# Kernel optimization log

Measured on AMD Instinct MI355X. Metric: run time of the kernel, lower is better.

The kernel has to match this reference:

```python
import jax, jax.numpy as jnp
import numpy as np

N_ITERS = 200  # matches maxIter=200 in the original QPFunction


def setup_inputs() -> dict:
    key = jax.random.key(0)
    k1, k2, k3 = jax.random.split(key, 3)
    B, M, N = 8192, 128, 64
    A = jax.random.normal(k1, (B, M, N), dtype=jnp.float32)
    x = jax.random.normal(k2, (B, N), dtype=jnp.float32)
    # b > 0 guarantees z = 0 is feasible for A z <= b, so every instance is solvable
    b = jax.random.uniform(k3, (B, M), dtype=jnp.float32)
    Q = jnp.eye(N, dtype=jnp.float32)  # module parameter: self.Q = diag(ones(feature_size))
    return {"Q": Q, "A": A, "x": x, "b": b}


def reference(Q, A, x, b):
    """Batched QP:  min_z 1/2 z^T Q z - x^T z  s.t.  A z <= b.

    Solved via FISTA (accelerated projected gradient ascent) on the dual:
        max_{lam >= 0}  -1/2 (x - A^T lam)^T Q^{-1} (x - A^T lam) - lam^T b + const
    Primal recovery: z = Q^{-1} (x - A^T lam).
    Fully batched and jit-friendly (fixed N_ITERS, lax.scan).
    """
    Qinv = jnp.linalg.inv(Q)  # [n, n], tiny

    # Lipschitz bound for dual gradient: ||A Qinv A^T||_2 <= ||A||_F^2 * ||Qinv||_F
    L = jnp.sum(A * A, axis=(1, 2)) * jnp.linalg.norm(Qinv)  # [B]
    eta = jax.lax.stop_gradient(1.0 / jnp.maximum(L, 1e-12))[:, None]  # [B, 1]

    def primal(lam):
        # z = Qinv (x - A^T lam), shape [B, n]
        return jnp.einsum('nk,bk->bn', Qinv, x - jnp.einsum('bmn,bm->bn', A, lam))

    def step(carry, _):
        lam, y, t = carry
        z = primal(y)                                   # [B, n]
        g = jnp.einsum('bmn,bn->bm', A, z) - b          # dual gradient A z - b, [B, m]
        lam_new = jax.nn.relu(y + eta * g)              # projected ascent step
        t_new = 0.5 * (1.0 + jnp.sqrt(1.0 + 4.0 * t * t))
        y_new = lam_new + ((t - 1.0) / t_new) * (lam_new - lam)
        return (lam_new, y_new, t_new), None

    lam0 = jnp.zeros_like(b)
    t0 = jnp.float32(1.0)
    (lam, _, _), _ = jax.lax.scan(step, (lam0, lam0, t0), None, length=N_ITERS)
    return primal(lam)  # optimal z, [B, n]
```

## Files before the change

kernel.cpp:

```cpp
#include <hip/hip_runtime.h>


constexpr double csqrt_(double x) {
  double g = x * 0.5 + 0.5;
  for (int i = 0; i < 40; ++i) g = 0.5 * (g + x / g);
  return g;
}
struct CoefT { float c[200]; };
constexpr CoefT make_coefs() {
  CoefT T{};
  double t = 1.0;
  for (int k = 0; k < 200; ++k) {
    double tn = 0.5 * (1.0 + csqrt_(1.0 + 4.0 * t * t));
    T.c[k] = (float)((t - 1.0) / tn);
    t = tn;
  }
  return T;
}
__device__ constexpr CoefT kCoef = make_coefs();

__device__ __forceinline__ float dpp_add_xor1(float v) {
  int r = __builtin_amdgcn_update_dpp(0, __float_as_int(v), 0xB1, 0xF, 0xF, true);
  return v + __int_as_float(r);
}
__device__ __forceinline__ float dpp_add_xor2(float v) {
  int r = __builtin_amdgcn_update_dpp(0, __float_as_int(v), 0x4E, 0xF, 0xF, true);
  return v + __int_as_float(r);
}
__device__ __forceinline__ float swz_add_xor4(float v) {
  int r = __builtin_amdgcn_ds_swizzle(__float_as_int(v), 0x101F);
  return v + __int_as_float(r);
}

__global__ __launch_bounds__(512)
void qp_fista_kernel(const float* __restrict__ A,
                     const float* __restrict__ x,
                     const float* __restrict__ b,
                     float* __restrict__ out) {
  const int batch = blockIdx.x;
  const int tid = threadIdx.x;
  const int w = tid >> 6;

  __shared__ __align__(16) float tile[8192];

  const float* Ag = A + (size_t)batch * 8192;

  {
    const float4* Ag4 = (const float4*)Ag;
    float4* t4 = (float4*)tile;
#pragma unroll
    for (int k = 0; k < 4; ++k) t4[tid + k * 512] = Ag4[tid + k * 512];
  }
  __syncthreads();

  const int r  = tid >> 2;
  const int cq = tid & 3;
  float Ar[16];
  {
    const float4* t4 = (const float4*)tile;
#pragma unroll
    for (int j = 0; j < 4; ++j) {
      float4 v = t4[r * 16 + cq * 4 + j];
      Ar[4 * j + 0] = v.x; Ar[4 * j + 1] = v.y;
      Ar[4 * j + 2] = v.z; Ar[4 * j + 3] = v.w;
    }
  }
  const int c  = tid >> 3;
  const int rq = tid & 7;
  float Ac[16];
#pragma unroll
  for (int i = 0; i < 16; ++i) Ac[i] = tile[(rq * 16 + i) * 64 + c];

  float ss = 0.f;
#pragma unroll
  for (int i = 0; i < 16; ++i) ss = fmaf(Ar[i], Ar[i], ss);
#pragma unroll
  for (int d = 1; d < 64; d <<= 1) ss += __shfl_xor(ss, d, 64);

  __syncthreads();

  float* zbuf = tile;
  float* ybuf = tile + 96;
  float* wsb  = tile + 272;

  if ((tid & 63) == 0) wsb[w] = ss;
  const float breg = b[(size_t)batch * 128 + r];
  const float xreg = x[(size_t)batch * 64 + c];
  if (rq == 0) zbuf[(c >> 4) * 20 + (c & 15)] = xreg;
  __syncthreads();

  float sum8 = 0.f;
#pragma unroll
  for (int i = 0; i < 8; ++i) sum8 += wsb[i];
  const float eta = 1.0f / fmaxf(8.0f * sum8, 1e-12f);
  const float yb0 = eta * breg;

  const float4* zs = (const float4*)(zbuf + cq * 20);
  const float4* ys = (const float4*)(ybuf + rq * 20);
  float* ywr = ybuf + w * 20 + (r & 15);
  float* zwr = zbuf + (c >> 4) * 20 + (c & 15);

  float lam = 0.f, y = 0.f;

#pragma unroll 2
  for (int it = 0; it < 199; ++it) {
    const float coef = kCoef.c[it];

    __builtin_amdgcn_s_setprio(1);
    float p0 = 0.f, p1 = 0.f;
#pragma unroll
    for (int j = 0; j < 4; ++j) {
      float4 zz = zs[j];
      p0 = fmaf(Ar[4 * j + 0], zz.x, p0);
      p1 = fmaf(Ar[4 * j + 1], zz.y, p1);
      p0 = fmaf(Ar[4 * j + 2], zz.z, p0);
      p1 = fmaf(Ar[4 * j + 3], zz.w, p1);
    }
    float acc = p0 + p1;
    acc = dpp_add_xor1(acc);
    acc = dpp_add_xor2(acc);
    float ln = fmaxf(0.f, fmaf(eta, acc, y - yb0));
    float yn = fmaf(coef, ln - lam, ln);
    __builtin_amdgcn_s_setprio(0);
    lam = ln; y = yn;
    if (cq == 0) *ywr = yn;
    __syncthreads();

    __builtin_amdgcn_s_setprio(1);
    float q0 = 0.f, q1 = 0.f;
#pragma unroll
    for (int j = 0; j < 4; ++j) {
      float4 yy = ys[j];
      q0 = fmaf(Ac[4 * j + 0], yy.x, q0);
      q1 = fmaf(Ac[4 * j + 1], yy.y, q1);
      q0 = fmaf(Ac[4 * j + 2], yy.z, q0);
      q1 = fmaf(Ac[4 * j + 3], yy.w, q1);
    }
    float s = q0 + q1;
    s = dpp_add_xor1(s);
    s = dpp_add_xor2(s);
    s = swz_add_xor4(s);
    __builtin_amdgcn_s_setprio(0);
    if (rq == 0) *zwr = xreg - s;
    __syncthreads();
  }

  {
    float p0 = 0.f, p1 = 0.f;
#pragma unroll
    for (int j = 0; j < 4; ++j) {
      float4 zz = zs[j];
      p0 = fmaf(Ar[4 * j + 0], zz.x, p0);
      p1 = fmaf(Ar[4 * j + 1], zz.y, p1);
      p0 = fmaf(Ar[4 * j + 2], zz.z, p0);
      p1 = fmaf(Ar[4 * j + 3], zz.w, p1);
    }
    float acc = p0 + p1;
    acc = dpp_add_xor1(acc);
    acc = dpp_add_xor2(acc);
    float ln = fmaxf(0.f, fmaf(eta, acc, y - yb0));
    if (cq == 0) *ywr = ln;
    __syncthreads();

    float q0 = 0.f, q1 = 0.f;
#pragma unroll
    for (int j = 0; j < 4; ++j) {
      float4 yy = ys[j];
      q0 = fmaf(Ac[4 * j + 0], yy.x, q0);
      q1 = fmaf(Ac[4 * j + 1], yy.y, q1);
      q0 = fmaf(Ac[4 * j + 2], yy.z, q0);
      q1 = fmaf(Ac[4 * j + 3], yy.w, q1);
    }
    float s = q0 + q1;
    s = dpp_add_xor1(s);
    s = dpp_add_xor2(s);
    s = swz_add_xor4(s);
    if (rq == 0) *zwr = xreg - s;
    __syncthreads();
  }

  if (tid < 64) {
    out[(size_t)batch * 64 + tid] = zbuf[(tid >> 4) * 20 + (tid & 15)];
  }
}

extern "C" void kernel_launch(void* const* d_in, const int* in_sizes, int n_in,
                              void* d_out, int out_size, void* d_ws, size_t ws_size,
                              hipStream_t stream) {
  const float* A = (const float*)d_in[1];
  const float* x = (const float*)d_in[2];
  const float* b = (const float*)d_in[3];
  float* out = (float*)d_out;
  qp_fista_kernel<<<dim3(8192), dim3(512), 0, stream>>>(A, x, b, out);
}
```

Measured before the change: 1.048 ms.

## Remap A*z phase to 4 rows x 4 cols per thread with transposed DPP reduction

Each thread in the A·z phase now holds a 4-row by 4-column sub-block of A instead of 16 columns of a single row. It needs only one float4 LDS read of z per iteration instead of four. The cross-lane reduction becomes a transpose-style butterfly using selects plus DPP xor1/xor2 and row-rotate 4/8, so each lane ends up with the full sum for its own row. The z buffer stride changes to 24 floats, presumably to avoid LDS bank conflicts. The aim is to cut LDS traffic per iteration, at the cost of a longer DPP reduction chain and extra select instructions.

```diff
diff --git a/kernel.cpp b/kernel.cpp
--- a/kernel.cpp
+++ b/kernel.cpp
@@ -19,13 +19,19 @@
 }
 __device__ constexpr CoefT kCoef = make_coefs();
 
-__device__ __forceinline__ float dpp_add_xor1(float v) {
-  int r = __builtin_amdgcn_update_dpp(0, __float_as_int(v), 0xB1, 0xF, 0xF, true);
-  return v + __int_as_float(r);
-}
-__device__ __forceinline__ float dpp_add_xor2(float v) {
-  int r = __builtin_amdgcn_update_dpp(0, __float_as_int(v), 0x4E, 0xF, 0xF, true);
-  return v + __int_as_float(r);
+__device__ __forceinline__ float dpp_xor1(float v) {
+  return __int_as_float(__builtin_amdgcn_update_dpp(0, __float_as_int(v), 0xB1, 0xF, 0xF, true));
+}
+__device__ __forceinline__ float dpp_xor2(float v) {
+  return __int_as_float(__builtin_amdgcn_update_dpp(0, __float_as_int(v), 0x4E, 0xF, 0xF, true));
+}
+__device__ __forceinline__ float dpp_add_xor1(float v) { return v + dpp_xor1(v); }
+__device__ __forceinline__ float dpp_add_xor2(float v) { return v + dpp_xor2(v); }
+__device__ __forceinline__ float dpp_add_ror4(float v) {
+  return v + __int_as_float(__builtin_amdgcn_update_dpp(0, __float_as_int(v), 0x124, 0xF, 0xF, true));
+}
+__device__ __forceinline__ float dpp_add_ror8(float v) {
+  return v + __int_as_float(__builtin_amdgcn_update_dpp(0, __float_as_int(v), 0x128, 0xF, 0xF, true));
 }
 __device__ __forceinline__ float swz_add_xor4(float v) {
   int r = __builtin_amdgcn_ds_swizzle(__float_as_int(v), 0x101F);
@@ -53,16 +59,16 @@
   }
   __syncthreads();
 
-  const int r  = tid >> 2;
-  const int cq = tid & 3;
-  float Ar[16];
+  const int rg = tid >> 4;
+  const int cs = tid & 15;
+  float Ar4[16];
   {
     const float4* t4 = (const float4*)tile;
 #pragma unroll
-    for (int j = 0; j < 4; ++j) {
-      float4 v = t4[r * 16 + cq * 4 + j];
-      Ar[4 * j + 0] = v.x; Ar[4 * j + 1] = v.y;
-      Ar[4 * j + 2] = v.z; Ar[4 * j + 3] = v.w;
+    for (int k = 0; k < 4; ++k) {
+      float4 v = t4[(4 * rg + k) * 16 + cs];
+      Ar4[4 * k + 0] = v.x; Ar4[4 * k + 1] = v.y;
+      Ar4[4 * k + 2] = v.z; Ar4[4 * k + 3] = v.w;
     }
   }
   const int c  = tid >> 3;
@@ -73,7 +79,7 @@
 
   float ss = 0.f;
 #pragma unroll
-  for (int i = 0; i < 16; ++i) ss = fmaf(Ar[i], Ar[i], ss);
+  for (int i = 0; i < 16; ++i) ss = fmaf(Ar4[i], Ar4[i], ss);
 #pragma unroll
   for (int d = 1; d < 64; d <<= 1) ss += __shfl_xor(ss, d, 64);
 
@@ -84,9 +90,10 @@
   float* wsb  = tile + 272;
 
   if ((tid & 63) == 0) wsb[w] = ss;
-  const float breg = b[(size_t)batch * 128 + r];
+  const int myrow = 4 * rg + (tid & 3);
+  const float breg = b[(size_t)batch * 128 + myrow];
   const float xreg = x[(size_t)batch * 64 + c];
-  if (rq == 0) zbuf[(c >> 4) * 20 + (c & 15)] = xreg;
+  if (rq == 0) zbuf[(c >> 4) * 24 + (c & 15)] = xreg;
   __syncthreads();
 
   float sum8 = 0.f;
@@ -95,10 +102,12 @@
   const float eta = 1.0f / fmaxf(8.0f * sum8, 1e-12f);
   const float yb0 = eta * breg;
 
-  const float4* zs = (const float4*)(zbuf + cq * 20);
+  const float4* zs = (const float4*)(zbuf + (cs >> 2) * 24 + (cs & 3) * 4);
   const float4* ys = (const float4*)(ybuf + rq * 20);
-  float* ywr = ybuf + w * 20 + (r & 15);
-  float* zwr = zbuf + (c >> 4) * 20 + (c & 15);
+  float* ywr = ybuf + w * 20 + 4 * (rg & 3) + (tid & 3);
+  const bool ywrite = ((tid & 12) == 0);
+  float* zwr = zbuf + (c >> 4) * 24 + (c & 15);
+  const bool sel0 = (tid & 1), sel1 = (tid & 2);
 
   float lam = 0.f, y = 0.f;
 
@@ -107,23 +116,27 @@
     const float coef = kCoef.c[it];
 
     __builtin_amdgcn_s_setprio(1);
-    float p0 = 0.f, p1 = 0.f;
-#pragma unroll
-    for (int j = 0; j < 4; ++j) {
-      float4 zz = zs[j];
-      p0 = fmaf(Ar[4 * j + 0], zz.x, p0);
-      p1 = fmaf(Ar[4 * j + 1], zz.y, p1);
-      p0 = fmaf(Ar[4 * j + 2], zz.z, p0);
-      p1 = fmaf(Ar[4 * j + 3], zz.w, p1);
-    }
-    float acc = p0 + p1;
-    acc = dpp_add_xor1(acc);
-    acc = dpp_add_xor2(acc);
-    float ln = fmaxf(0.f, fmaf(eta, acc, y - yb0));
+    float4 zz = *zs;
+    float a0 = Ar4[0] * zz.x, a1 = Ar4[4] * zz.x, a2 = Ar4[8] * zz.x, a3 = Ar4[12] * zz.x;
+    a0 = fmaf(Ar4[1], zz.y, a0);  a1 = fmaf(Ar4[5], zz.y, a1);
+    a2 = fmaf(Ar4[9], zz.y, a2);  a3 = fmaf(Ar4[13], zz.y, a3);
+    a0 = fmaf(Ar4[2], zz.z, a0);  a1 = fmaf(Ar4[6], zz.z, a1);
+    a2 = fmaf(Ar4[10], zz.z, a2); a3 = fmaf(Ar4[14], zz.z, a3);
+    a0 = fmaf(Ar4[3], zz.w, a0);  a1 = fmaf(Ar4[7], zz.w, a1);
+    a2 = fmaf(Ar4[11], zz.w, a2); a3 = fmaf(Ar4[15], zz.w, a3);
+    float u01 = sel0 ? a1 : a0, v01 = sel0 ? a0 : a1;
+    u01 += dpp_xor1(v01);
+    float u23 = sel0 ? a3 : a2, v23 = sel0 ? a2 : a3;
+    u23 += dpp_xor1(v23);
+    float s2 = sel1 ? u23 : u01, t2 = sel1 ? u01 : u23;
+    s2 += dpp_xor2(t2);
+    s2 = dpp_add_ror4(s2);
+    s2 = dpp_add_ror8(s2);
+    float ln = fmaxf(0.f, fmaf(eta, s2, y - yb0));
     float yn = fmaf(coef, ln - lam, ln);
     __builtin_amdgcn_s_setprio(0);
     lam = ln; y = yn;
-    if (cq == 0) *ywr = yn;
+    if (ywrite) *ywr = yn;
     __syncthreads();
 
     __builtin_amdgcn_s_setprio(1);
@@ -146,20 +159,24 @@
   }
 
   {
-    float p0 = 0.f, p1 = 0.f;
-#pragma unroll
-    for (int j = 0; j < 4; ++j) {
-      float4 zz = zs[j];
-      p0 = fmaf(Ar[4 * j + 0], zz.x, p0);
-      p1 = fmaf(Ar[4 * j + 1], zz.y, p1);
-      p0 = fmaf(Ar[4 * j + 2], zz.z, p0);
-      p1 = fmaf(Ar[4 * j + 3], zz.w, p1);
-    }
-    float acc = p0 + p1;
-    acc = dpp_add_xor1(acc);
-    acc = dpp_add_xor2(acc);
-    float ln = fmaxf(0.f, fmaf(eta, acc, y - yb0));
-    if (cq == 0) *ywr = ln;
+    float4 zz = *zs;
+    float a0 = Ar4[0] * zz.x, a1 = Ar4[4] * zz.x, a2 = Ar4[8] * zz.x, a3 = Ar4[12] * zz.x;
+    a0 = fmaf(Ar4[1], zz.y, a0);  a1 = fmaf(Ar4[5], zz.y, a1);
+    a2 = fmaf(Ar4[9], zz.y, a2);  a3 = fmaf(Ar4[13], zz.y, a3);
+    a0 = fmaf(Ar4[2], zz.z, a0);  a1 = fmaf(Ar4[6], zz.z, a1);
+    a2 = fmaf(Ar4[10], zz.z, a2); a3 = fmaf(Ar4[14], zz.z, a3);
+    a0 = fmaf(Ar4[3], zz.w, a0);  a1 = fmaf(Ar4[7], zz.w, a1);
+    a2 = fmaf(Ar4[11], zz.w, a2); a3 = fmaf(Ar4[15], zz.w, a3);
+    float u01 = sel0 ? a1 : a0, v01 = sel0 ? a0 : a1;
+    u01 += dpp_xor1(v01);
+    float u23 = sel0 ? a3 : a2, v23 = sel0 ? a2 : a3;
+    u23 += dpp_xor1(v23);
+    float s2 = sel1 ? u23 : u01, t2 = sel1 ? u01 : u23;
+    s2 += dpp_xor2(t2);
+    s2 = dpp_add_ror4(s2);
+    s2 = dpp_add_ror8(s2);
+    float ln = fmaxf(0.f, fmaf(eta, s2, y - yb0));
+    if (ywrite) *ywr = ln;
     __syncthreads();
 
     float q0 = 0.f, q1 = 0.f;
@@ -180,7 +197,7 @@
   }
 
   if (tid < 64) {
-    out[(size_t)batch * 64 + tid] = zbuf[(tid >> 4) * 20 + (tid & 15)];
+    out[(size_t)batch * 64 + tid] = zbuf[(tid >> 4) * 24 + (tid & 15)];
   }
 }
 
```

Result: faster. 1.001 ms (-4.5%).
